# Kernel optimization log

Measured on AMD Instinct MI355X. Metric: run time of the kernel, lower is better.

Reference implementation:

```python
import jax, jax.numpy as jnp
import numpy as np

T, B, H, N2 = 4096, 2, 2048, 8  # seq_len, batch, embed_dim, ndim//2 complex modes


def setup_inputs() -> dict:
    key = jax.random.key(0)
    k1, k2, k3, k4, k5 = jax.random.split(key, 5)
    x = jax.random.normal(k1, (T, B, H), dtype=jnp.float32)
    D_param = jax.random.normal(k2, (H,), dtype=jnp.float32)
    # dt log-uniform in [1e-3, 1e-1] (standard S4D init)
    u = jax.random.uniform(k3, (H,), dtype=jnp.float32)
    log_dt = u * (jnp.log(0.1) - jnp.log(0.001)) + jnp.log(0.001)
    # S4D-Lin init: A = -1/2 + i*pi*n
    A_real_log = jnp.full((H, N2), jnp.log(0.5), dtype=jnp.float32)
    A_imag = jnp.broadcast_to(np.pi * jnp.arange(N2, dtype=jnp.float32), (H, N2))
    C_re = jax.random.normal(k4, (H, N2), dtype=jnp.float32)
    C_im = jax.random.normal(k5, (H, N2), dtype=jnp.float32)
    return {"x": x, "D_param": D_param, "log_dt": log_dt,
            "A_real_log": A_real_log, "A_imag": A_imag,
            "C_re": C_re, "C_im": C_im}


def _s4d_kernel(log_dt, A_real_log, A_imag, C_re, C_im, L):
    # Diagonal SSM (S4D, ZOH-style) convolution kernel, shape (H, L)
    dt = jnp.exp(log_dt)[:, None]                      # (H, 1)
    A = -jnp.exp(A_real_log) + 1j * A_imag             # (H, N2) complex64
    dtA = A * dt                                       # (H, N2)
    C = (C_re + 1j * C_im) * (jnp.exp(dtA) - 1.0) / A  # discretized C
    vander = jnp.exp(dtA[:, :, None] * jnp.arange(L))  # (H, N2, L)
    return 2.0 * jnp.einsum('hn,hnl->hl', C, vander).real


def reference(x, D_param, log_dt, A_real_log, A_imag, C_re, C_im):
    seq_len = x.shape[0]
    residual = x * D_param                     # (T, B, H)
    xb = jnp.transpose(x, (1, 2, 0))           # (B, H, T)
    k = _s4d_kernel(log_dt, A_real_log, A_imag, C_re, C_im, seq_len)  # (H, T)
    n = 2 * seq_len
    k_f = jnp.fft.rfft(k, n=n)                 # (H, T+1) complex
    x_f = jnp.fft.rfft(xb, n=n)                # (B, H, T+1)
    out = jnp.fft.irfft(x_f * k_f, n=n)[..., :seq_len]  # (B, H, T)
    return jnp.transpose(out, (2, 0, 1)) + residual      # (T, B, H)
```

## Files before the change

### kernel.cpp

```cpp
#include <hip/hip_runtime.h>

#define T_LEN 4096
#define B_SZ  2
#define H_SZ  2048
#define NM    8
#define BH    (B_SZ * H_SZ)


template <int LC>
__global__ void __launch_bounds__(256, 4)
k1_chunk_end(const float* __restrict__ x,
             const float* __restrict__ log_dt,
             const float* __restrict__ Arl,
             const float* __restrict__ Aimp,
             float2* __restrict__ states) {
    int g = blockIdx.x * blockDim.x + threadIdx.x;
    int h = g % H_SZ;
    int b = (g / H_SZ) % B_SZ;
    int c = g / BH;

    float dt = __expf(log_dt[h]);
    float wr[NM], wi[NM];
#pragma unroll
    for (int n = 0; n < NM; ++n) {
        float ar  = -__expf(Arl[h * NM + n]);
        float ai  = Aimp[h * NM + n];
        float er  = __expf(ar * dt);
        float ang = ai * dt;
        wr[n] = er * __cosf(ang);
        wi[n] = er * __sinf(ang);
    }

    float sr[NM], si[NM];
#pragma unroll
    for (int n = 0; n < NM; ++n) { sr[n] = 0.f; si[n] = 0.f; }

    const float* xp = x + (size_t)c * LC * BH + b * H_SZ + h;

    constexpr int BT = 8;
    float buf[BT], nxt[BT];
#pragma unroll
    for (int i = 0; i < BT; ++i) buf[i] = xp[(size_t)i * BH];

#pragma unroll
    for (int tb = 0; tb < LC / BT; ++tb) {
        if (tb + 1 < LC / BT) {
#pragma unroll
            for (int i = 0; i < BT; ++i)
                nxt[i] = xp[(size_t)((tb + 1) * BT + i) * BH];
        }
#pragma unroll
        for (int i = 0; i < BT; ++i) {
            float xv = buf[i];
#pragma unroll
            for (int n = 0; n < NM; ++n) {
                float nsr = fmaf(wr[n], sr[n], fmaf(-wi[n], si[n], xv));
                float nsi = fmaf(wr[n], si[n], wi[n] * sr[n]);
                sr[n] = nsr; si[n] = nsi;
            }
        }
#pragma unroll
        for (int i = 0; i < BT; ++i) buf[i] = nxt[i];
    }

    float2* st = states + (size_t)(c * B_SZ + b) * NM * H_SZ + h;
#pragma unroll
    for (int n = 0; n < NM; ++n) st[(size_t)n * H_SZ] = make_float2(sr[n], si[n]);
}

template <int CC, int LC>
__global__ void __launch_bounds__(256, 4)
k2_carry_scan(const float* __restrict__ log_dt,
              const float* __restrict__ Arl,
              const float* __restrict__ Aimp,
              float2* __restrict__ states) {
    int g = blockIdx.x * blockDim.x + threadIdx.x;
    int h = g % H_SZ;
    int n = (g / H_SZ) % NM;
    int b = g / (H_SZ * NM);

    float dt  = __expf(log_dt[h]);
    float Are = -__expf(Arl[h * NM + n]);
    float Aim = Aimp[h * NM + n];
    float er  = __expf(Are * dt * (float)LC);
    float ang = Aim * dt * (float)LC;
    float wr = er * __cosf(ang), wi = er * __sinf(ang);

    const size_t stride = (size_t)B_SZ * NM * H_SZ;
    float2* base = states + ((size_t)b * NM + n) * H_SZ + h;

    float cr = 0.f, ci = 0.f;
    constexpr int BT = 8;
    float2 buf[BT], nxt[BT];
#pragma unroll
    for (int i = 0; i < BT; ++i) buf[i] = base[(size_t)i * stride];

#pragma unroll
    for (int cb = 0; cb < CC / BT; ++cb) {
        if (cb + 1 < CC / BT) {
#pragma unroll
            for (int i = 0; i < BT; ++i)
                nxt[i] = base[(size_t)((cb + 1) * BT + i) * stride];
        }
#pragma unroll
        for (int i = 0; i < BT; ++i) {
            int c = cb * BT + i;
            base[(size_t)c * stride] = make_float2(cr, ci);
            float ncr = fmaf(wr, cr, fmaf(-wi, ci, buf[i].x));
            float nci = fmaf(wr, ci, fmaf(wi, cr, buf[i].y));
            cr = ncr; ci = nci;
        }
#pragma unroll
        for (int i = 0; i < BT; ++i) buf[i] = nxt[i];
    }
}

template <int LC>
__global__ void __launch_bounds__(256, 4)
k3_output(const float* __restrict__ x,
          const float* __restrict__ Dp,
          const float* __restrict__ log_dt,
          const float* __restrict__ Arl,
          const float* __restrict__ Aimp,
          const float* __restrict__ Crep,
          const float* __restrict__ Cimp,
          const float2* __restrict__ states,
          float* __restrict__ out) {
    int g = blockIdx.x * blockDim.x + threadIdx.x;
    int h = g % H_SZ;
    int b = (g / H_SZ) % B_SZ;
    int c = g / BH;

    float dt = __expf(log_dt[h]);
    float wr[NM], wi[NM], cdr[NM], cdi[NM];
#pragma unroll
    for (int n = 0; n < NM; ++n) {
        float ar  = -__expf(Arl[h * NM + n]);
        float ai  = Aimp[h * NM + n];
        float er  = __expf(ar * dt);
        float ang = ai * dt;
        float wrn = er * __cosf(ang);
        float win = er * __sinf(ang);
        wr[n] = wrn; wi[n] = win;
        float inv = 1.0f / (ar * ar + ai * ai);
        float tr = ((wrn - 1.f) * ar + win * ai) * inv;
        float ti = (win * ar - (wrn - 1.f) * ai) * inv;
        float Cre = Crep[h * NM + n], Cim = Cimp[h * NM + n];
        cdr[n] = Cre * tr - Cim * ti;
        cdi[n] = Cre * ti + Cim * tr;
    }

    const float2* st = states + (size_t)(c * B_SZ + b) * NM * H_SZ + h;
    float sr[NM], si[NM];
#pragma unroll
    for (int n = 0; n < NM; ++n) {
        float2 v = st[(size_t)n * H_SZ];
        sr[n] = v.x; si[n] = v.y;
    }

    float Dv = Dp[h];
    const float* xp = x + (size_t)c * LC * BH + b * H_SZ + h;
    float* op = out + (size_t)c * LC * BH + b * H_SZ + h;

    constexpr int BT = 8;
    float buf[BT], nxt[BT];
#pragma unroll
    for (int i = 0; i < BT; ++i) buf[i] = xp[(size_t)i * BH];

#pragma unroll
    for (int tb = 0; tb < LC / BT; ++tb) {
        if (tb + 1 < LC / BT) {
#pragma unroll
            for (int i = 0; i < BT; ++i)
                nxt[i] = xp[(size_t)((tb + 1) * BT + i) * BH];
        }
#pragma unroll
        for (int i = 0; i < BT; ++i) {
            float xv = buf[i];
            float y = 0.f;
#pragma unroll
            for (int n = 0; n < NM; ++n) {
                float nsr = fmaf(wr[n], sr[n], fmaf(-wi[n], si[n], xv));
                float nsi = fmaf(wr[n], si[n], wi[n] * sr[n]);
                sr[n] = nsr; si[n] = nsi;
                y = fmaf(cdr[n], nsr, y);
                y = fmaf(-cdi[n], nsi, y);
            }
            float ov = fmaf(Dv, xv, 2.0f * y);
            __builtin_nontemporal_store(ov, op + (size_t)(tb * BT + i) * BH);
        }
#pragma unroll
        for (int i = 0; i < BT; ++i) buf[i] = nxt[i];
    }
}

extern "C" void kernel_launch(void* const* d_in, const int* in_sizes, int n_in,
                              void* d_out, int out_size, void* d_ws, size_t ws_size,
                              hipStream_t stream) {
    const float* x      = (const float*)d_in[0];
    const float* Dp     = (const float*)d_in[1];
    const float* log_dt = (const float*)d_in[2];
    const float* Arl    = (const float*)d_in[3];
    const float* Aimp   = (const float*)d_in[4];
    const float* Cre    = (const float*)d_in[5];
    const float* Cim    = (const float*)d_in[6];
    float* out = (float*)d_out;
    float2* states = (float2*)d_ws;

    const size_t need64 = (size_t)64 * BH * NM * sizeof(float2);

    if (ws_size >= need64) {
        constexpr int C = 64, LC = T_LEN / 64;
        int total1 = C * BH;
        k1_chunk_end<LC><<<total1 / 256, 256, 0, stream>>>(x, log_dt, Arl, Aimp, states);
        int total2 = BH * NM;
        k2_carry_scan<C, LC><<<total2 / 256, 256, 0, stream>>>(log_dt, Arl, Aimp, states);
        k3_output<LC><<<total1 / 256, 256, 0, stream>>>(x, Dp, log_dt, Arl, Aimp,
                                                        Cre, Cim, states, out);
    } else {
        constexpr int C = 32, LC = T_LEN / 32;
        int total1 = C * BH;
        k1_chunk_end<LC><<<total1 / 256, 256, 0, stream>>>(x, log_dt, Arl, Aimp, states);
        int total2 = BH * NM;
        k2_carry_scan<C, LC><<<total2 / 256, 256, 0, stream>>>(log_dt, Arl, Aimp, states);
        k3_output<LC><<<total1 / 256, 256, 0, stream>>>(x, Dp, log_dt, Arl, Aimp,
                                                        Cre, Cim, states, out);
    }
}
```

Before: 154.1 us.

## Fuse chunk scan, carry scan and output into one cooperative kernel

Replaces the three-kernel chunked scan with a single cooperative launch that uses grid-wide syncs between the chunk-end state pass, the carry scan over chunks, and the output pass. It also switches to 32 chunks and deeper load prefetch, and keeps per-thread decay factors in registers across phases. The aim is to remove launch gaps and recomputation. In exchange, the grid of 512 blocks must be fully co-resident (otherwise it falls back to the old kernels), and fewer chunks means longer serial loops with less parallelism.

```diff
diff --git a/kernel.cpp b/kernel.cpp
--- a/kernel.cpp
+++ b/kernel.cpp
@@ -1,10 +1,176 @@
 #include <hip/hip_runtime.h>
+#include <hip/hip_cooperative_groups.h>
+
+namespace cg = cooperative_groups;
 
 #define T_LEN 4096
 #define B_SZ  2
 #define H_SZ  2048
 #define NM    8
 #define BH    (B_SZ * H_SZ)
+
+
+template <int C, int LC, int BT>
+__global__ void __launch_bounds__(256, 4)
+s4d_fused(const float* __restrict__ x,
+          const float* __restrict__ Dp,
+          const float* __restrict__ log_dt,
+          const float* __restrict__ Arl,
+          const float* __restrict__ Aimp,
+          const float* __restrict__ Crep,
+          const float* __restrict__ Cimp,
+          float2* __restrict__ states,
+          float* __restrict__ out) {
+    cg::grid_group grid = cg::this_grid();
+
+    const int g = blockIdx.x * blockDim.x + threadIdx.x;
+    const int h = g % H_SZ;
+    const int b = (g / H_SZ) % B_SZ;
+    const int c = g / BH;
+
+    const float dt = __expf(log_dt[h]);
+    float wr[NM], wi[NM];
+#pragma unroll
+    for (int n = 0; n < NM; ++n) {
+        float ar  = -__expf(Arl[h * NM + n]);
+        float ai  = Aimp[h * NM + n];
+        float er  = __expf(ar * dt);
+        float ang = ai * dt;
+        wr[n] = er * __cosf(ang);
+        wi[n] = er * __sinf(ang);
+    }
+
+    {
+        float sr[NM], si[NM];
+#pragma unroll
+        for (int n = 0; n < NM; ++n) { sr[n] = 0.f; si[n] = 0.f; }
+
+        const float* xp = x + (size_t)c * LC * BH + b * H_SZ + h;
+        float buf[BT], nxt[BT];
+#pragma unroll
+        for (int i = 0; i < BT; ++i) buf[i] = xp[(size_t)i * BH];
+
+#pragma unroll
+        for (int tb = 0; tb < LC / BT; ++tb) {
+            if (tb + 1 < LC / BT) {
+#pragma unroll
+                for (int i = 0; i < BT; ++i)
+                    nxt[i] = xp[(size_t)((tb + 1) * BT + i) * BH];
+            }
+#pragma unroll
+            for (int i = 0; i < BT; ++i) {
+                float xv = buf[i];
+#pragma unroll
+                for (int n = 0; n < NM; ++n) {
+                    float nsr = fmaf(wr[n], sr[n], fmaf(-wi[n], si[n], xv));
+                    float nsi = fmaf(wr[n], si[n], wi[n] * sr[n]);
+                    sr[n] = nsr; si[n] = nsi;
+                }
+            }
+#pragma unroll
+            for (int i = 0; i < BT; ++i) buf[i] = nxt[i];
+        }
+
+        float2* st = states + (size_t)(c * B_SZ + b) * NM * H_SZ + h;
+#pragma unroll
+        for (int n = 0; n < NM; ++n)
+            st[(size_t)n * H_SZ] = make_float2(sr[n], si[n]);
+    }
+
+    __threadfence();
+    grid.sync();
+    __threadfence();
+
+    if (g < BH * NM) {
+        const int h2 = g % H_SZ;
+        const int n2 = (g / H_SZ) % NM;
+        const int b2 = g / (H_SZ * NM);
+
+        float dt2 = __expf(log_dt[h2]);
+        float Are = -__expf(Arl[h2 * NM + n2]);
+        float Aim = Aimp[h2 * NM + n2];
+        float er  = __expf(Are * dt2 * (float)LC);
+        float ang = Aim * dt2 * (float)LC;
+        float cwr = er * __cosf(ang), cwi = er * __sinf(ang);
+
+        const size_t stride = (size_t)B_SZ * NM * H_SZ;
+        float2* base = states + ((size_t)b2 * NM + n2) * H_SZ + h2;
+
+        float2 v[C];
+#pragma unroll
+        for (int i = 0; i < C; ++i) v[i] = base[(size_t)i * stride];
+
+        float cr = 0.f, ci = 0.f;
+#pragma unroll
+        for (int i = 0; i < C; ++i) {
+            base[(size_t)i * stride] = make_float2(cr, ci);
+            float ncr = fmaf(cwr, cr, fmaf(-cwi, ci, v[i].x));
+            float nci = fmaf(cwr, ci, fmaf(cwi, cr, v[i].y));
+            cr = ncr; ci = nci;
+        }
+    }
+
+    __threadfence();
+    grid.sync();
+    __threadfence();
+
+    {
+        float cdr[NM], cdi[NM];
+#pragma unroll
+        for (int n = 0; n < NM; ++n) {
+            float ar  = -__expf(Arl[h * NM + n]);
+            float ai  = Aimp[h * NM + n];
+            float inv = 1.0f / (ar * ar + ai * ai);
+            float tr = ((wr[n] - 1.f) * ar + wi[n] * ai) * inv;
+            float ti = (wi[n] * ar - (wr[n] - 1.f) * ai) * inv;
+            float Cre = Crep[h * NM + n], Cim = Cimp[h * NM + n];
+            cdr[n] = Cre * tr - Cim * ti;
+            cdi[n] = Cre * ti + Cim * tr;
+        }
+
+        const float2* st = states + (size_t)(c * B_SZ + b) * NM * H_SZ + h;
+        float sr[NM], si[NM];
+#pragma unroll
+        for (int n = 0; n < NM; ++n) {
+            float2 v2 = st[(size_t)n * H_SZ];
+            sr[n] = v2.x; si[n] = v2.y;
+        }
+
+        float Dv = Dp[h];
+        const float* xp = x + (size_t)c * LC * BH + b * H_SZ + h;
+        float* op = out + (size_t)c * LC * BH + b * H_SZ + h;
+
+        float buf[BT], nxt[BT];
+#pragma unroll
+        for (int i = 0; i < BT; ++i) buf[i] = xp[(size_t)i * BH];
+
+#pragma unroll
+        for (int tb = 0; tb < LC / BT; ++tb) {
+            if (tb + 1 < LC / BT) {
+#pragma unroll
+                for (int i = 0; i < BT; ++i)
+                    nxt[i] = xp[(size_t)((tb + 1) * BT + i) * BH];
+            }
+#pragma unroll
+            for (int i = 0; i < BT; ++i) {
+                float xv = buf[i];
+                float y = 0.f;
+#pragma unroll
+                for (int n = 0; n < NM; ++n) {
+                    float nsr = fmaf(wr[n], sr[n], fmaf(-wi[n], si[n], xv));
+                    float nsi = fmaf(wr[n], si[n], wi[n] * sr[n]);
+                    sr[n] = nsr; si[n] = nsi;
+                    y = fmaf(cdr[n], nsr, y);
+                    y = fmaf(-cdi[n], nsi, y);
+                }
+                __builtin_nontemporal_store(fmaf(Dv, xv, 2.0f * y),
+                                            op + (size_t)(tb * BT + i) * BH);
+            }
+#pragma unroll
+            for (int i = 0; i < BT; ++i) buf[i] = nxt[i];
+        }
+    }
+}
 
 
 template <int LC>
@@ -207,23 +373,42 @@
     float* out = (float*)d_out;
     float2* states = (float2*)d_ws;
 
-    const size_t need64 = (size_t)64 * BH * NM * sizeof(float2);
-
-    if (ws_size >= need64) {
-        constexpr int C = 64, LC = T_LEN / 64;
-        int total1 = C * BH;
-        k1_chunk_end<LC><<<total1 / 256, 256, 0, stream>>>(x, log_dt, Arl, Aimp, states);
-        int total2 = BH * NM;
-        k2_carry_scan<C, LC><<<total2 / 256, 256, 0, stream>>>(log_dt, Arl, Aimp, states);
-        k3_output<LC><<<total1 / 256, 256, 0, stream>>>(x, Dp, log_dt, Arl, Aimp,
-                                                        Cre, Cim, states, out);
-    } else {
-        constexpr int C = 32, LC = T_LEN / 32;
-        int total1 = C * BH;
-        k1_chunk_end<LC><<<total1 / 256, 256, 0, stream>>>(x, log_dt, Arl, Aimp, states);
-        int total2 = BH * NM;
-        k2_carry_scan<C, LC><<<total2 / 256, 256, 0, stream>>>(log_dt, Arl, Aimp, states);
-        k3_output<LC><<<total1 / 256, 256, 0, stream>>>(x, Dp, log_dt, Arl, Aimp,
-                                                        Cre, Cim, states, out);
+    constexpr int C  = 32;
+    constexpr int LC = T_LEN / C;
+    constexpr int BT = 16;
+    const size_t need = (size_t)C * BH * NM * sizeof(float2);
+
+    bool fused_ok = false;
+    if (ws_size >= need) {
+        int blocks = C * BH / 256;
+        void* args[] = {(void*)&x, (void*)&Dp, (void*)&log_dt, (void*)&Arl,
+                        (void*)&Aimp, (void*)&Cre, (void*)&Cim,
+                        (void*)&states, (void*)&out};
+        hipError_t e = hipLaunchCooperativeKernel(
+            reinterpret_cast<void*>(&s4d_fused<C, LC, BT>),
+            dim3(blocks), dim3(256), args, 0, stream);
+        fused_ok = (e == hipSuccess);
+        if (!fused_ok) (void)hipGetLastError();
+    }
+
+    if (!fused_ok) {
+        const size_t need64 = (size_t)64 * BH * NM * sizeof(float2);
+        if (ws_size >= need64) {
+            constexpr int Cf = 64, LCf = T_LEN / 64;
+            int total1 = Cf * BH;
+            k1_chunk_end<LCf><<<total1 / 256, 256, 0, stream>>>(x, log_dt, Arl, Aimp, states);
+            int total2 = BH * NM;
+            k2_carry_scan<Cf, LCf><<<total2 / 256, 256, 0, stream>>>(log_dt, Arl, Aimp, states);
+            k3_output<LCf><<<total1 / 256, 256, 0, stream>>>(x, Dp, log_dt, Arl, Aimp,
+                                                             Cre, Cim, states, out);
+        } else {
+            constexpr int Cf = 32, LCf = T_LEN / 32;
+            int total1 = Cf * BH;
+            k1_chunk_end<LCf><<<total1 / 256, 256, 0, stream>>>(x, log_dt, Arl, Aimp, states);
+            int total2 = BH * NM;
+            k2_carry_scan<Cf, LCf><<<total2 / 256, 256, 0, stream>>>(log_dt, Arl, Aimp, states);
+            k3_output<LCf><<<total1 / 256, 256, 0, stream>>>(x, Dp, log_dt, Arl, Aimp,
+                                                             Cre, Cim, states, out);
+        }
     }
 }
```

New measurement: 515.7 us. +234.8%, slower.
